# Performance work log

Measured on AMD Instinct MI355X. Metric: run time of the kernel, lower is better.

Reference implementation:

```python
import jax, jax.numpy as jnp
import numpy as np

NHEAD = 16
NUM_GROUPS = 4
EXPERTS_PER_GROUP = 2
LN_EPS = 1e-5


def _layernorm(x, g, b):
    mu = jnp.mean(x, axis=-1, keepdims=True)
    var = jnp.mean(jnp.square(x - mu), axis=-1, keepdims=True)
    return (x - mu) * jax.lax.rsqrt(var + LN_EPS) * g + b


def _mha(x, wi, bi, wo, bo):
    # torch nn.MultiheadAttention (batch_first): qkv = x @ in_proj_w.T + in_proj_b
    B, S, D = x.shape
    hd = D // NHEAD
    qkv = x @ wi.T + bi                      # [B,S,3D]
    q, k, v = jnp.split(qkv, 3, axis=-1)
    def heads(t):
        return t.reshape(B, S, NHEAD, hd).transpose(0, 2, 1, 3)  # [B,H,S,hd]
    q, k, v = heads(q), heads(k), heads(v)
    scores = jnp.einsum('bhqd,bhkd->bhqk', q, k) / jnp.sqrt(jnp.asarray(hd, x.dtype))
    attn = jax.nn.softmax(scores, axis=-1)
    o = jnp.einsum('bhqk,bhkd->bhqd', attn, v)
    o = o.transpose(0, 2, 1, 3).reshape(B, S, D)
    return o @ wo.T + bo


def _hier_moe(x, w_group, b_group, w_expert, b_expert, w1, b1, w2, b2):
    # Two-level top-1 routing: group gate -> expert gate within chosen group.
    B, S, D = x.shape
    xt = x.reshape(B * S, D)                 # [T,D]
    T = xt.shape[0]
    E = NUM_GROUPS * EXPERTS_PER_GROUP

    gp = jax.nn.softmax(xt @ w_group + b_group, axis=-1)          # [T,G]
    g_idx = jnp.argmax(gp, axis=-1)                                # [T]
    g_prob = jnp.max(gp, axis=-1)                                  # [T]

    elog = jnp.einsum('td,gde->tge', xt, w_expert) + b_expert      # [T,G,Epg]
    ep = jax.nn.softmax(elog, axis=-1)
    ep_sel = jnp.take_along_axis(ep, g_idx[:, None, None], axis=1)[:, 0, :]  # [T,Epg]
    e_idx_local = jnp.argmax(ep_sel, axis=-1)                      # [T]
    e_prob = jnp.max(ep_sel, axis=-1)                              # [T]

    flat_e = g_idx * EXPERTS_PER_GROUP + e_idx_local               # [T]
    combine = jax.nn.one_hot(flat_e, E, dtype=xt.dtype) * (g_prob * e_prob)[:, None]  # [T,E]

    # Dense dispatch (reference): run every expert on all tokens, combine with one-hot weights.
    h = jax.nn.relu(jnp.einsum('td,edf->etf', xt, w1) + b1[:, None, :])   # [E,T,Fff]
    y = jnp.einsum('etf,efd->etd', h, w2) + b2[:, None, :]                # [E,T,D]
    out = jnp.einsum('te,etd->td', combine, y)                            # [T,D]
    return out.reshape(B, S, D)


def setup_inputs() -> dict:
    key = jax.random.key(0)
    ks = jax.random.split(key, 8)
    B, S, D, F = 2, 1024, 1024, 2048
    G, Epg = NUM_GROUPS, EXPERTS_PER_GROUP
    E = G * Epg
    sc = lambda fan: 1.0 / np.sqrt(fan)
    return {
        'x': jax.random.normal(ks[0], (B, S, D), jnp.float32),
        'in_proj_w': jax.random.normal(ks[1], (3 * D, D), jnp.float32) * sc(D),
        'in_proj_b': jnp.zeros((3 * D,), jnp.float32),
        'out_proj_w': jax.random.normal(ks[2], (D, D), jnp.float32) * sc(D),
        'out_proj_b': jnp.zeros((D,), jnp.float32),
        'ln1_g': jnp.ones((D,), jnp.float32),
        'ln1_b': jnp.zeros((D,), jnp.float32),
        'ln2_g': jnp.ones((D,), jnp.float32),
        'ln2_b': jnp.zeros((D,), jnp.float32),
        'w_group': jax.random.normal(ks[3], (D, G), jnp.float32) * sc(D),
        'b_group': jnp.zeros((G,), jnp.float32),
        'w_expert': jax.random.normal(ks[4], (G, D, Epg), jnp.float32) * sc(D),
        'b_expert': jnp.zeros((G, Epg), jnp.float32),
        'w1': jax.random.normal(ks[5], (E, D, F), jnp.float32) * sc(D),
        'b1': jnp.zeros((E, F), jnp.float32),
        'w2': jax.random.normal(ks[6], (E, F, D), jnp.float32) * sc(F),
        'b2': jnp.zeros((E, D), jnp.float32),
    }


def reference(x, in_proj_w, in_proj_b, out_proj_w, out_proj_b,
              ln1_g, ln1_b, ln2_g, ln2_b,
              w_group, b_group, w_expert, b_expert, w1, b1, w2, b2):
    # Dropout p=0.1 is identity in eval mode.
    attn_out = _mha(x, in_proj_w, in_proj_b, out_proj_w, out_proj_b)
    x = _layernorm(x + attn_out, ln1_g, ln1_b)
    moe_out = _hier_moe(x, w_group, b_group, w_expert, b_expert, w1, b1, w2, b2)
    x = _layernorm(x + moe_out, ln2_g, ln2_b)
    return x
```

## Files before the change

### kernel.cpp

```cpp
#include <hip/hip_runtime.h>
#include <hip/hip_bf16.h>

#define TT 2048
#define DD 1024
#define FF 2048
#define SS 1024
#define NHD 16
#define HDD 64
#define NG 4
#define EPG 2
#define NE 8

#define QSC 0.18033688011112042f

typedef __attribute__((ext_vector_type(8))) short bf16x8;
typedef __attribute__((ext_vector_type(4))) float f32x4;
typedef __attribute__((ext_vector_type(4))) unsigned short ush4;

__device__ __forceinline__ unsigned short f2bf(float x) {
    unsigned int u = __float_as_uint(x);
    u = (u + 0x7fffu + ((u >> 16) & 1u)) >> 16;
    return (unsigned short)u;
}
__device__ __forceinline__ float bf2f(unsigned short h) {
    return __uint_as_float((unsigned int)h << 16);
}

__device__ __forceinline__ float wave_sum(float s) {
#pragma unroll
    for (int off = 32; off > 0; off >>= 1) s += __shfl_xor(s, off);
    return s;
}

__device__ __forceinline__ void gl16(const void* g, void* l) {
    auto gp = reinterpret_cast<const unsigned int __attribute__((address_space(1)))*>(
        (unsigned long long)g);
    auto lp = reinterpret_cast<unsigned int __attribute__((address_space(3)))*>(
        (unsigned int)(unsigned long long)l);
    __builtin_amdgcn_global_load_lds(gp, lp, 16, 0, 0);
}

__global__ __launch_bounds__(256) void split_bf16_kernel(
    const float* __restrict__ in, unsigned short* __restrict__ hi,
    unsigned short* __restrict__ lo, int n4)
{
    const int i = blockIdx.x * 256 + threadIdx.x;
    if (i >= n4) return;
    const float4 v = ((const float4*)in)[i];
    float vv[4] = {v.x, v.y, v.z, v.w};
    ush4 h, l;
#pragma unroll
    for (int j = 0; j < 4; ++j) {
        const unsigned short hb = f2bf(vv[j]);
        ((unsigned short*)&h)[j] = hb;
        ((unsigned short*)&l)[j] = f2bf(vv[j] - bf2f(hb));
    }
    ((ush4*)hi)[i] = h;
    ((ush4*)lo)[i] = l;
}

__global__ __launch_bounds__(256, 3) void gemm_split_kernel(
    const unsigned short* __restrict__ Ah, const unsigned short* __restrict__ Al,
    const unsigned short* __restrict__ Bh, const unsigned short* __restrict__ Bl,
    const float* __restrict__ bias, const float* __restrict__ resid,
    float* __restrict__ C, unsigned short* __restrict__ Chi,
    unsigned short* __restrict__ Clo, int qscale_n, int M, int N, int K)
{
    __shared__ unsigned short sAh[128 * 64];
    __shared__ unsigned short sAl[128 * 64];
    __shared__ unsigned short sBh[64 * 64];
    __shared__ unsigned short sBl[64 * 64];
    const int tid = threadIdx.x;
    const int lane = tid & 63, wid = tid >> 6;
    const int l15 = lane & 15, lg = lane >> 4;
    const int n0 = blockIdx.x << 6, m0 = blockIdx.y << 7;

    f32x4 acc[2][4];
#pragma unroll
    for (int mi = 0; mi < 2; ++mi)
#pragma unroll
        for (int ni = 0; ni < 4; ++ni) acc[mi][ni] = (f32x4){0.f, 0.f, 0.f, 0.f};

    for (int k0 = 0; k0 < K; k0 += 64) {
#pragma unroll
        for (int r = 0; r < 4; ++r) {
            const int s = (r << 8) + tid;
            const int row = s >> 3;
            const int cs = (s & 7) ^ (row & 7);
            const int lb = (s & ~63) << 3;
            const size_t ga = (size_t)(m0 + row) * K + k0 + (cs << 3);
            gl16(Ah + ga, &sAh[lb]);
            gl16(Al + ga, &sAl[lb]);
        }
#pragma unroll
        for (int r = 0; r < 2; ++r) {
            const int s = (r << 8) + tid;
            const int row = s >> 3;
            const int cs = (s & 7) ^ (row & 7);
            const int lb = (s & ~63) << 3;
            const size_t gb = (size_t)(n0 + row) * K + k0 + (cs << 3);
            gl16(Bh + gb, &sBh[lb]);
            gl16(Bl + gb, &sBl[lb]);
        }
        __syncthreads();
#pragma unroll
        for (int ks = 0; ks < 2; ++ks) {
            bf16x8 ah[2], al[2], bh[4], bl[4];
            const int ac = (ks << 2) + lg;
#pragma unroll
            for (int i = 0; i < 2; ++i) {
                const int ar = (wid << 5) + (i << 4) + l15;
                const int pa = ((ar << 3) | (ac ^ (ar & 7))) << 3;
                ah[i] = *(const bf16x8*)&sAh[pa];
                al[i] = *(const bf16x8*)&sAl[pa];
            }
#pragma unroll
            for (int i = 0; i < 4; ++i) {
                const int br = (i << 4) + l15;
                const int pb = ((br << 3) | (ac ^ (br & 7))) << 3;
                bh[i] = *(const bf16x8*)&sBh[pb];
                bl[i] = *(const bf16x8*)&sBl[pb];
            }
#pragma unroll
            for (int mi = 0; mi < 2; ++mi)
#pragma unroll
                for (int ni = 0; ni < 4; ++ni) {
                    acc[mi][ni] = __builtin_amdgcn_mfma_f32_16x16x32_bf16(ah[mi], bh[ni], acc[mi][ni], 0, 0, 0);
                    acc[mi][ni] = __builtin_amdgcn_mfma_f32_16x16x32_bf16(ah[mi], bl[ni], acc[mi][ni], 0, 0, 0);
                    acc[mi][ni] = __builtin_amdgcn_mfma_f32_16x16x32_bf16(al[mi], bh[ni], acc[mi][ni], 0, 0, 0);
                }
        }
        __syncthreads();
    }
#pragma unroll
    for (int mi = 0; mi < 2; ++mi)
#pragma unroll
        for (int ni = 0; ni < 4; ++ni)
#pragma unroll
            for (int r2 = 0; r2 < 4; ++r2) {
                const int m = m0 + (wid << 5) + (mi << 4) + (lg << 2) + r2;
                const int n = n0 + (ni << 4) + l15;
                float v = acc[mi][ni][r2] + bias[n];
                if (resid) v += resid[(size_t)m * N + n];
                const size_t idx = (size_t)m * N + n;
                if (Chi) {
                    if (n < qscale_n) v *= QSC;
                    const unsigned short hb = f2bf(v);
                    Chi[idx] = hb;
                    Clo[idx] = f2bf(v - bf2f(hb));
                } else {
                    C[idx] = v;
                }
            }
}

__global__ __launch_bounds__(256) void vtrans_kernel(
    const unsigned short* __restrict__ src, unsigned short* __restrict__ dst)
{
    __shared__ unsigned short tile[64][65];
    const int bh = blockIdx.y, b = bh >> 4, h = bh & 15;
    const int s0 = blockIdx.x << 6;
    const int tid = threadIdx.x;
#pragma unroll
    for (int r = 0; r < 2; ++r) {
        const int sl = tid + (r << 8);
        const int rr = sl >> 3, c8 = (sl & 7) << 3;
        const bf16x8 v = *(const bf16x8*)(src + (size_t)(b * SS + s0 + rr) * 3072 + 2048 + h * HDD + c8);
#pragma unroll
        for (int j = 0; j < 8; ++j) tile[rr][c8 + j] = ((const unsigned short*)&v)[j];
    }
    __syncthreads();
#pragma unroll
    for (int r = 0; r < 2; ++r) {
        const int sl = tid + (r << 8);
        const int d = sl >> 3, s8 = (sl & 7) << 3;
        bf16x8 o;
#pragma unroll
        for (int j = 0; j < 8; ++j) ((unsigned short*)&o)[j] = tile[s8 + j][d];
        *(bf16x8*)(dst + (size_t)(bh * HDD + d) * SS + s0 + s8) = o;
    }
}

__global__ __launch_bounds__(256, 4) void attn_mfma_kernel(
    const unsigned short* __restrict__ qh, const unsigned short* __restrict__ ql,
    const unsigned short* __restrict__ vth, const unsigned short* __restrict__ vtl,
    float* __restrict__ opart, float* __restrict__ mpart, float* __restrict__ lpart)
{
    __shared__ unsigned short sKh[4096], sKl[4096];
    __shared__ unsigned short sVh[4096], sVl[4096];
    const int bh = blockIdx.y, b = bh >> 4, h = bh & 15;
    const int q0 = blockIdx.x << 6;
    const int z = blockIdx.z;
    const int tid = threadIdx.x, lane = tid & 63, w = tid >> 6;
    const int l15 = lane & 15, lg = lane >> 4;

#pragma unroll
    for (int r = 0; r < 2; ++r) {
        const int s = (r << 8) + tid;
        const int row = s >> 3;
        const int cs = (s & 7) ^ (row & 7);
        const int lb = (s & ~63) << 3;
        const size_t gq = (size_t)(b * SS + q0 + row) * 3072 + h * HDD + (cs << 3);
        gl16(qh + gq, &sKh[lb]);
        gl16(ql + gq, &sKl[lb]);
    }
    __syncthreads();
    bf16x8 qah[2], qal[2];
#pragma unroll
    for (int ks = 0; ks < 2; ++ks) {
        const int ar = (w << 4) + l15;
        const int ac = (ks << 2) + lg;
        const int pa = ((ar << 3) | (ac ^ (ar & 7))) << 3;
        qah[ks] = *(const bf16x8*)&sKh[pa];
        qal[ks] = *(const bf16x8*)&sKl[pa];
    }
    __syncthreads();

    f32x4 accO[4];
#pragma unroll
    for (int nt = 0; nt < 4; ++nt) accO[nt] = (f32x4){0.f, 0.f, 0.f, 0.f};
    float m_run[4], l_run[4];
#pragma unroll
    for (int r2 = 0; r2 < 4; ++r2) { m_run[r2] = -3.0e38f; l_run[r2] = 0.f; }

    const int kvbeg = z << 9;
    for (int kv0 = kvbeg; kv0 < kvbeg + 512; kv0 += 64) {
#pragma unroll
        for (int r = 0; r < 2; ++r) {
            const int s = (r << 8) + tid;
            const int row = s >> 3;
            const int cs = (s & 7) ^ (row & 7);
            const int lb = (s & ~63) << 3;
            const size_t gk = (size_t)(b * SS + kv0 + row) * 3072 + DD + h * HDD + (cs << 3);
            gl16(qh + gk, &sKh[lb]);
            gl16(ql + gk, &sKl[lb]);
            const size_t gv = (size_t)(bh * HDD + row) * SS + kv0 + (cs << 3);
            gl16(vth + gv, &sVh[lb]);
            gl16(vtl + gv, &sVl[lb]);
        }
        __syncthreads();

        f32x4 sacc[4];
#pragma unroll
        for (int i = 0; i < 4; ++i) sacc[i] = (f32x4){0.f, 0.f, 0.f, 0.f};
        __builtin_amdgcn_s_setprio(1);
#pragma unroll
        for (int ks = 0; ks < 2; ++ks) {
            const int ac = (ks << 2) + lg;
#pragma unroll
            for (int i = 0; i < 4; ++i) {
                const int br = (i << 4) + l15;
                const int pb = ((br << 3) | (ac ^ (br & 7))) << 3;
                const bf16x8 kbh = *(const bf16x8*)&sKh[pb];
                const bf16x8 kbl = *(const bf16x8*)&sKl[pb];
                sacc[i] = __builtin_amdgcn_mfma_f32_16x16x32_bf16(qah[ks], kbh, sacc[i], 0, 0, 0);
                sacc[i] = __builtin_amdgcn_mfma_f32_16x16x32_bf16(qah[ks], kbl, sacc[i], 0, 0, 0);
                sacc[i] = __builtin_amdgcn_mfma_f32_16x16x32_bf16(qal[ks], kbh, sacc[i], 0, 0, 0);
            }
        }
        __builtin_amdgcn_s_setprio(0);
        __syncthreads();

#pragma unroll
        for (int r2 = 0; r2 < 4; ++r2) {
            float mx = fmaxf(fmaxf(sacc[0][r2], sacc[1][r2]), fmaxf(sacc[2][r2], sacc[3][r2]));
#pragma unroll
            for (int off = 1; off < 16; off <<= 1) mx = fmaxf(mx, __shfl_xor(mx, off));
            const float mn = fmaxf(m_run[r2], mx);
            const float corr = exp2f(m_run[r2] - mn);
            m_run[r2] = mn;
            float ls = 0.f;
#pragma unroll
            for (int nt = 0; nt < 4; ++nt) {
                const float p = exp2f(sacc[nt][r2] - mn);
                sacc[nt][r2] = p;
                ls += p;
            }
#pragma unroll
            for (int off = 1; off < 16; off <<= 1) ls += __shfl_xor(ls, off);
            l_run[r2] = l_run[r2] * corr + ls;
#pragma unroll
            for (int nt = 0; nt < 4; ++nt) accO[nt][r2] *= corr;
        }

#pragma unroll
        for (int nt = 0; nt < 4; ++nt)
#pragma unroll
            for (int r2 = 0; r2 < 4; ++r2) {
                const int qq = (w << 4) + (lg << 2) + r2;
                const int kv = (nt << 4) + l15;
                const int idx = (qq << 6) + ((((kv >> 3) ^ (qq & 7))) << 3) + (kv & 7);
                const float p = sacc[nt][r2];
                const unsigned short hb = (unsigned short)(__float_as_uint(p) >> 16);
                sKh[idx] = hb;
                sKl[idx] = (unsigned short)(__float_as_uint(p - bf2f(hb)) >> 16);
            }

        __builtin_amdgcn_s_setprio(1);
#pragma unroll
        for (int ks = 0; ks < 2; ++ks) {
            const int qq = (w << 4) + l15;
            const int slot = (ks << 2) + lg;
            const int pidx = (qq << 6) + ((slot ^ (qq & 7)) << 3);
            const bf16x8 pah = *(const bf16x8*)&sKh[pidx];
            const bf16x8 pal = *(const bf16x8*)&sKl[pidx];
            const int ac = (ks << 2) + lg;
#pragma unroll
            for (int nt = 0; nt < 4; ++nt) {
                const int dr = (nt << 4) + l15;
                const int pv = ((dr << 3) | (ac ^ (dr & 7))) << 3;
                const bf16x8 vbh = *(const bf16x8*)&sVh[pv];
                const bf16x8 vbl = *(const bf16x8*)&sVl[pv];
                accO[nt] = __builtin_amdgcn_mfma_f32_16x16x32_bf16(pah, vbh, accO[nt], 0, 0, 0);
                accO[nt] = __builtin_amdgcn_mfma_f32_16x16x32_bf16(pah, vbl, accO[nt], 0, 0, 0);
                accO[nt] = __builtin_amdgcn_mfma_f32_16x16x32_bf16(pal, vbh, accO[nt], 0, 0, 0);
            }
        }
        __builtin_amdgcn_s_setprio(0);
        __syncthreads();
    }

#pragma unroll
    for (int nt = 0; nt < 4; ++nt)
#pragma unroll
        for (int r2 = 0; r2 < 4; ++r2) {
            const int qq = q0 + (w << 4) + (lg << 2) + r2;
            const int dd = h * HDD + (nt << 4) + l15;
            opart[((size_t)z * TT + b * SS + qq) * DD + dd] = accO[nt][r2];
        }
    if (l15 == 0) {
#pragma unroll
        for (int r2 = 0; r2 < 4; ++r2) {
            const int qq = q0 + (w << 4) + (lg << 2) + r2;
            const int idx = z * (32 * SS) + bh * SS + qq;
            mpart[idx] = m_run[r2];
            lpart[idx] = l_run[r2];
        }
    }
}

__global__ __launch_bounds__(256) void attn_combine_kernel(
    const float* __restrict__ opart, const float* __restrict__ mpart,
    const float* __restrict__ lpart, unsigned short* __restrict__ ohi,
    unsigned short* __restrict__ olo)
{
    const int t = blockIdx.x;
    const int tid = threadIdx.x;
    const int b = t >> 10, q = t & 1023;
    const int d0 = tid << 2;
    const int bh = (b << 4) + (d0 >> 6);
    const int mi = bh * SS + q;
    const float m0 = mpart[mi], m1 = mpart[32 * SS + mi];
    const float l0 = lpart[mi], l1 = lpart[32 * SS + mi];
    const float m = fmaxf(m0, m1);
    const float e0 = exp2f(m0 - m), e1 = exp2f(m1 - m);
    const float inv = 1.0f / (l0 * e0 + l1 * e1);
    const float4 a = *(const float4*)(opart + (size_t)t * DD + d0);
    const float4 c = *(const float4*)(opart + (size_t)(TT + t) * DD + d0);
    const float vv[4] = { (a.x * e0 + c.x * e1) * inv, (a.y * e0 + c.y * e1) * inv,
                          (a.z * e0 + c.z * e1) * inv, (a.w * e0 + c.w * e1) * inv };
    ush4 hh, ll;
#pragma unroll
    for (int j = 0; j < 4; ++j) {
        const unsigned short hb = f2bf(vv[j]);
        hh[j] = hb;
        ll[j] = f2bf(vv[j] - bf2f(hb));
    }
    *(ush4*)(ohi + (size_t)t * DD + d0) = hh;
    *(ush4*)(olo + (size_t)t * DD + d0) = ll;
}

__global__ __launch_bounds__(256) void ln_kernel(
    const float* __restrict__ in, const float* __restrict__ gamma,
    const float* __restrict__ beta, float* __restrict__ outf)
{
    const int t = blockIdx.x;
    const int tid = threadIdx.x;
    __shared__ float red[8];
    const float4 v = ((const float4*)(in + (size_t)t * DD))[tid];
    float s = v.x + v.y + v.z + v.w;
    s = wave_sum(s);
    const int wid = tid >> 6, lane = tid & 63;
    if (lane == 0) red[wid] = s;
    __syncthreads();
    const float mu = (red[0] + red[1] + red[2] + red[3]) * (1.0f / DD);
    const float d0 = v.x - mu, d1 = v.y - mu, d2 = v.z - mu, d3 = v.w - mu;
    float q = d0 * d0 + d1 * d1 + d2 * d2 + d3 * d3;
    q = wave_sum(q);
    if (lane == 0) red[4 + wid] = q;
    __syncthreads();
    const float var = (red[4] + red[5] + red[6] + red[7]) * (1.0f / DD);
    const float rstd = 1.0f / sqrtf(var + 1e-5f);
    const float4 g4 = ((const float4*)gamma)[tid];
    const float4 b4 = ((const float4*)beta)[tid];
    float4 ov = { d0 * rstd * g4.x + b4.x, d1 * rstd * g4.y + b4.y,
                  d2 * rstd * g4.z + b4.z, d3 * rstd * g4.w + b4.w };
    ((float4*)(outf + (size_t)t * DD))[tid] = ov;
}

__global__ __launch_bounds__(256) void ln_route_kernel(
    const float* __restrict__ in, const float* __restrict__ gamma,
    const float* __restrict__ beta, float* __restrict__ outf,
    unsigned short* __restrict__ outb,
    const float* __restrict__ wg, const float* __restrict__ bg,
    const float* __restrict__ we, const float* __restrict__ be,
    int* __restrict__ eid, float* __restrict__ gate, int* __restrict__ counts)
{
    const int t = blockIdx.x;
    const int tid = threadIdx.x;
    __shared__ float red[8];
    __shared__ float red2[4][12];
    const float4 v = ((const float4*)(in + (size_t)t * DD))[tid];
    float s = v.x + v.y + v.z + v.w;
    s = wave_sum(s);
    const int wid = tid >> 6, lane = tid & 63;
    if (lane == 0) red[wid] = s;
    __syncthreads();
    const float mu = (red[0] + red[1] + red[2] + red[3]) * (1.0f / DD);
    const float d0 = v.x - mu, d1 = v.y - mu, d2 = v.z - mu, d3 = v.w - mu;
    float q = d0 * d0 + d1 * d1 + d2 * d2 + d3 * d3;
    q = wave_sum(q);
    if (lane == 0) red[4 + wid] = q;
    __syncthreads();
    const float var = (red[4] + red[5] + red[6] + red[7]) * (1.0f / DD);
    const float rstd = 1.0f / sqrtf(var + 1e-5f);
    const float4 g4 = ((const float4*)gamma)[tid];
    const float4 b4 = ((const float4*)beta)[tid];
    const float o0 = d0 * rstd * g4.x + b4.x;
    const float o1 = d1 * rstd * g4.y + b4.y;
    const float o2 = d2 * rstd * g4.z + b4.z;
    const float o3 = d3 * rstd * g4.w + b4.w;
    float4 ov = {o0, o1, o2, o3};
    ((float4*)(outf + (size_t)t * DD))[tid] = ov;
    ush4 wv = { f2bf(o0), f2bf(o1), f2bf(o2), f2bf(o3) };
    *(ush4*)(outb + (size_t)t * DD + (tid << 2)) = wv;

    float pz[12];
#pragma unroll
    for (int k = 0; k < 12; ++k) pz[k] = 0.f;
    const float xo[4] = {o0, o1, o2, o3};
#pragma unroll
    for (int j = 0; j < 4; ++j) {
        const int c = (tid << 2) + j;
        const float xv = xo[j];
        const float4 wgv = *(const float4*)(wg + c * NG);
        pz[0] = fmaf(xv, wgv.x, pz[0]);
        pz[1] = fmaf(xv, wgv.y, pz[1]);
        pz[2] = fmaf(xv, wgv.z, pz[2]);
        pz[3] = fmaf(xv, wgv.w, pz[3]);
#pragma unroll
        for (int g = 0; g < NG; ++g) {
            const float2 wev = *(const float2*)(we + ((size_t)g * DD + c) * EPG);
            pz[4 + 2 * g]     = fmaf(xv, wev.x, pz[4 + 2 * g]);
            pz[4 + 2 * g + 1] = fmaf(xv, wev.y, pz[4 + 2 * g + 1]);
        }
    }
#pragma unroll
    for (int k = 0; k < 12; ++k) pz[k] = wave_sum(pz[k]);
    if (lane == 0) {
#pragma unroll
        for (int k = 0; k < 12; ++k) red2[wid][k] = pz[k];
    }
    __syncthreads();
    if (tid == 0) {
        float zs[12];
#pragma unroll
        for (int k = 0; k < 12; ++k)
            zs[k] = red2[0][k] + red2[1][k] + red2[2][k] + red2[3][k];
        float z[NG];
#pragma unroll
        for (int g = 0; g < NG; ++g) z[g] = zs[g] + bg[g];
        int gi = 0; float zb = z[0];
#pragma unroll
        for (int g = 1; g < NG; ++g) if (z[g] > zb) { zb = z[g]; gi = g; }
        float se = 0.f;
#pragma unroll
        for (int g = 0; g < NG; ++g) se += __expf(z[g] - zb);
        const float gprob = 1.0f / se;
        float e0 = 0.f, e1 = 0.f;
#pragma unroll
        for (int g = 0; g < NG; ++g) {
            if (g == gi) {
                e0 = zs[4 + 2 * g] + be[g * EPG + 0];
                e1 = zs[4 + 2 * g + 1] + be[g * EPG + 1];
            }
        }
        const int ei = (e1 > e0) ? 1 : 0;
        const float ehi = ei ? e1 : e0, elo = ei ? e0 : e1;
        const float eprob = 1.0f / (1.0f + __expf(elo - ehi));
        eid[t] = gi * EPG + ei;
        gate[t] = gprob * eprob;
        atomicAdd(&counts[gi * EPG + ei], 1);
    }
}

__global__ void zero_counts_kernel(int* __restrict__ counts) {
    if (threadIdx.x < NE) counts[threadIdx.x] = 0;
}

__global__ void offsets_kernel(const int* __restrict__ counts, int* __restrict__ offs,
                               int* __restrict__ cursor) {
    if (threadIdx.x == 0) {
        int run = 0;
        for (int e = 0; e < NE; ++e) { offs[e] = run; cursor[e] = run; run += counts[e]; }
        offs[NE] = run;
    }
}

__global__ __launch_bounds__(256) void scatter_kernel(const int* __restrict__ eid,
                                                      int* __restrict__ cursor,
                                                      int* __restrict__ perm) {
    const int t = blockIdx.x * 256 + threadIdx.x;
    const int slot = atomicAdd(&cursor[eid[t]], 1);
    perm[slot] = t;
}

__global__ __launch_bounds__(256) void transpose_bf16_kernel(
    const float* __restrict__ in, unsigned short* __restrict__ out, int R, int C)
{
    __shared__ float tile[32][33];
    const int c0 = blockIdx.x << 5, r0 = blockIdx.y << 5;
    const size_t bo = (size_t)blockIdx.z * R * C;
    const int tc = threadIdx.x & 31, tr8 = threadIdx.x >> 5;
#pragma unroll
    for (int p = 0; p < 4; ++p) {
        const int rr = tr8 + (p << 3);
        tile[rr][tc] = in[bo + (size_t)(r0 + rr) * C + c0 + tc];
    }
    __syncthreads();
#pragma unroll
    for (int p = 0; p < 4; ++p) {
        const int rr = tr8 + (p << 3);
        out[bo + (size_t)(c0 + rr) * R + r0 + tc] = f2bf(tile[tc][rr]);
    }
}

__global__ __launch_bounds__(256, 4) void moe_gemm1_kernel(
    const unsigned short* __restrict__ x1b, const unsigned short* __restrict__ w1t,
    const float* __restrict__ b1, const int* __restrict__ offs,
    const int* __restrict__ perm, unsigned short* __restrict__ hbuf)
{
    const int e = blockIdx.y >> 5, mt = blockIdx.y & 31;
    const int row0 = offs[e] + (mt << 6);
    const int rend = offs[e + 1];
    if (row0 >= rend) return;
    const int valid = min(rend - row0, 64);
    const int n0 = blockIdx.x << 6;
    __shared__ unsigned short sA[2][64 * 64];
    __shared__ unsigned short sB[2][64 * 64];
    const int tid = threadIdx.x;
    const int lane = tid & 63, w = tid >> 6;
    const int l15 = lane & 15, lg = lane >> 4;

    size_t abase[2], bbase[2];
    int lbs[2];
#pragma unroll
    for (int r = 0; r < 2; ++r) {
        const int s = (r << 8) + tid;
        const int row = s >> 3;
        const int cs = (s & 7) ^ (row & 7);
        lbs[r] = (s & ~63) << 3;
        const int tk = perm[min(row0 + row, rend - 1)];
        abase[r] = (size_t)tk * DD + (cs << 3);
        bbase[r] = ((size_t)e * FF + n0 + row) * DD + (cs << 3);
    }

    f32x4 acc[4];
#pragma unroll
    for (int nt = 0; nt < 4; ++nt) acc[nt] = (f32x4){0.f, 0.f, 0.f, 0.f};

#pragma unroll
    for (int r = 0; r < 2; ++r) {
        gl16(x1b + abase[r], &sA[0][lbs[r]]);
        gl16(w1t + bbase[r], &sB[0][lbs[r]]);
    }
    __syncthreads();
    int cur = 0;
    for (int k0 = 0; k0 < DD; k0 += 64) {
        const int nxt = k0 + 64;
        if (nxt < DD) {
#pragma unroll
            for (int r = 0; r < 2; ++r) {
                gl16(x1b + abase[r] + nxt, &sA[cur ^ 1][lbs[r]]);
                gl16(w1t + bbase[r] + nxt, &sB[cur ^ 1][lbs[r]]);
            }
        }
#pragma unroll
        for (int ks = 0; ks < 2; ++ks) {
            const int ac = (ks << 2) + lg;
            const int ar = (w << 4) + l15;
            const int pa = ((ar << 3) | (ac ^ (ar & 7))) << 3;
            const bf16x8 a = *(const bf16x8*)&sA[cur][pa];
#pragma unroll
            for (int nt = 0; nt < 4; ++nt) {
                const int br = (nt << 4) + l15;
                const int pb = ((br << 3) | (ac ^ (br & 7))) << 3;
                acc[nt] = __builtin_amdgcn_mfma_f32_16x16x32_bf16(
                    a, *(const bf16x8*)&sB[cur][pb], acc[nt], 0, 0, 0);
            }
        }
        __syncthreads();
        cur ^= 1;
    }

    const float* bias = b1 + e * FF + n0;
    const int mbase = (w << 4) + (lg << 2);
#pragma unroll
    for (int nt = 0; nt < 4; ++nt) {
        const int n = (nt << 4) + l15;
#pragma unroll
        for (int r2 = 0; r2 < 4; ++r2) {
            const int m = mbase + r2;
            if (m < valid) {
                float v = fmaxf(acc[nt][r2] + bias[n], 0.f);
                hbuf[(size_t)(row0 + m) * FF + n0 + n] = f2bf(v);
            }
        }
    }
}

__global__ __launch_bounds__(256, 4) void moe_gemm2_kernel(
    const unsigned short* __restrict__ hbuf, const unsigned short* __restrict__ w2t,
    const int* __restrict__ offs, float* __restrict__ p0, float* __restrict__ p1)
{
    const int e = blockIdx.y >> 5, mt = blockIdx.y & 31;
    const int row0 = offs[e] + (mt << 6);
    const int rend = offs[e + 1];
    if (row0 >= rend) return;
    const int valid = min(rend - row0, 64);
    const int n0 = blockIdx.x << 6;
    const int z = blockIdx.z;
    float* __restrict__ pbuf = z ? p1 : p0;
    __shared__ unsigned short sA[2][64 * 64];
    __shared__ unsigned short sB[2][64 * 64];
    const int tid = threadIdx.x;
    const int lane = tid & 63, w = tid >> 6;
    const int l15 = lane & 15, lg = lane >> 4;

    size_t abase[2], bbase[2];
    int lbs[2];
#pragma unroll
    for (int r = 0; r < 2; ++r) {
        const int s = (r << 8) + tid;
        const int row = s >> 3;
        const int cs = (s & 7) ^ (row & 7);
        lbs[r] = (s & ~63) << 3;
        abase[r] = (size_t)(row0 + row) * FF + (cs << 3);
        bbase[r] = ((size_t)e * DD + n0 + row) * FF + (cs << 3);
    }

    f32x4 acc[4];
#pragma unroll
    for (int nt = 0; nt < 4; ++nt) acc[nt] = (f32x4){0.f, 0.f, 0.f, 0.f};

    const int kbeg = z << 10, kend = kbeg + 1024;
#pragma unroll
    for (int r = 0; r < 2; ++r) {
        gl16(hbuf + abase[r] + kbeg, &sA[0][lbs[r]]);
        gl16(w2t + bbase[r] + kbeg, &sB[0][lbs[r]]);
    }
    __syncthreads();
    int cur = 0;
    for (int k0 = kbeg; k0 < kend; k0 += 64) {
        const int nxt = k0 + 64;
        if (nxt < kend) {
#pragma unroll
            for (int r = 0; r < 2; ++r) {
                gl16(hbuf + abase[r] + nxt, &sA[cur ^ 1][lbs[r]]);
                gl16(w2t + bbase[r] + nxt, &sB[cur ^ 1][lbs[r]]);
            }
        }
#pragma unroll
        for (int ks = 0; ks < 2; ++ks) {
            const int ac = (ks << 2) + lg;
            const int ar = (w << 4) + l15;
            const int pa = ((ar << 3) | (ac ^ (ar & 7))) << 3;
            const bf16x8 a = *(const bf16x8*)&sA[cur][pa];
#pragma unroll
            for (int nt = 0; nt < 4; ++nt) {
                const int br = (nt << 4) + l15;
                const int pb = ((br << 3) | (ac ^ (br & 7))) << 3;
                acc[nt] = __builtin_amdgcn_mfma_f32_16x16x32_bf16(
                    a, *(const bf16x8*)&sB[cur][pb], acc[nt], 0, 0, 0);
            }
        }
        __syncthreads();
        cur ^= 1;
    }

    const int mbase = (w << 4) + (lg << 2);
#pragma unroll
    for (int nt = 0; nt < 4; ++nt) {
        const int n = (nt << 4) + l15;
#pragma unroll
        for (int r2 = 0; r2 < 4; ++r2) {
            const int m = mbase + r2;
            if (m < valid) pbuf[(size_t)(row0 + m) * DD + n0 + n] = acc[nt][r2];
        }
    }
}

__global__ __launch_bounds__(256) void moe2_combine_kernel(
    const float* __restrict__ p0, const float* __restrict__ p1,
    const int* __restrict__ offs, const int* __restrict__ perm,
    const float* __restrict__ gate, const float* __restrict__ b2,
    const float* __restrict__ x1, float* __restrict__ res2)
{
    const int s = blockIdx.x;
    const int tid = threadIdx.x;
    int e = 0;
#pragma unroll
    for (int g = 1; g < NE; ++g) e += (s >= offs[g]) ? 1 : 0;
    const int tk = perm[s];
    const float gt = gate[tk];
    const int c0 = tid << 2;
    const float4 a  = *(const float4*)(p0 + (size_t)s * DD + c0);
    const float4 b  = *(const float4*)(p1 + (size_t)s * DD + c0);
    const float4 bb = *(const float4*)(b2 + (size_t)e * DD + c0);
    const float4 xx = *(const float4*)(x1 + (size_t)tk * DD + c0);
    float4 o = { xx.x + gt * (a.x + b.x + bb.x), xx.y + gt * (a.y + b.y + bb.y),
                 xx.z + gt * (a.z + b.z + bb.z), xx.w + gt * (a.w + b.w + bb.w) };
    *(float4*)(res2 + (size_t)tk * DD + c0) = o;
}

extern "C" void kernel_launch(void* const* d_in, const int* in_sizes, int n_in,
                              void* d_out, int out_size, void* d_ws, size_t ws_size,
                              hipStream_t stream)
{
    (void)in_sizes; (void)n_in; (void)out_size; (void)ws_size;
    const float* x   = (const float*)d_in[0];
    const float* wi  = (const float*)d_in[1];
    const float* bi  = (const float*)d_in[2];
    const float* wo  = (const float*)d_in[3];
    const float* bo  = (const float*)d_in[4];
    const float* g1  = (const float*)d_in[5];
    const float* be1 = (const float*)d_in[6];
    const float* g2  = (const float*)d_in[7];
    const float* be2 = (const float*)d_in[8];
    const float* wgr = (const float*)d_in[9];
    const float* bgr = (const float*)d_in[10];
    const float* wex = (const float*)d_in[11];
    const float* bex = (const float*)d_in[12];
    const float* w1  = (const float*)d_in[13];
    const float* b1  = (const float*)d_in[14];
    const float* w2  = (const float*)d_in[15];
    const float* b2  = (const float*)d_in[16];
    float* out = (float*)d_out;

    char* ws = (char*)d_ws;
    unsigned short* qkvh  = (unsigned short*)(ws + 0);
    unsigned short* qkvl  = (unsigned short*)(ws + 12582912);
    unsigned short* hbuf  = (unsigned short*)(ws + 0);
    float* res2           = (float*)(ws + 8388608);
    unsigned short* vth   = (unsigned short*)(ws + 25165824);
    unsigned short* vtl   = (unsigned short*)(ws + 29360128);
    float* res1           = (float*)(ws + 33554432);
    float* x1             = (float*)(ws + 41943040);
    unsigned short* x1b   = (unsigned short*)(ws + 50331648);
    unsigned short* w1t   = (unsigned short*)(ws + 54525952);
    unsigned short* w2t   = (unsigned short*)(ws + 88080384);
    char* misc = ws + 121634816;
    int*   eid    = (int*)(misc);
    float* gate   = (float*)(misc + 8192);
    int*   perm   = (int*)(misc + 16384);
    int*   counts = (int*)(misc + 24576);
    int*   offs   = (int*)(misc + 24640);
    int*   cursor = (int*)(misc + 24704);

    unsigned short* xs_hi = (unsigned short*)(ws + 33554432);
    unsigned short* xs_lo = (unsigned short*)(ws + 33554432 + 4194304);
    unsigned short* wi_hi = (unsigned short*)(ws + 54525952);
    unsigned short* wi_lo = (unsigned short*)(ws + 54525952 + 6291456);
    unsigned short* o_hi  = (unsigned short*)(ws + 41943040);
    unsigned short* o_lo  = (unsigned short*)(ws + 41943040 + 4194304);
    unsigned short* wo_hi = (unsigned short*)(ws + 88080384);
    unsigned short* wo_lo = (unsigned short*)(ws + 88080384 + 2097152);

    float* opart = (float*)(ws + 54525952);
    float* mpart = (float*)(ws + 54525952 + 16777216);
    float* lpart = (float*)(ws + 54525952 + 17039360);

    float* mp0 = (float*)(ws + 16777216);
    float* mp1 = (float*)(ws + 25165824);

    zero_counts_kernel<<<dim3(1), dim3(64), 0, stream>>>(counts);

    split_bf16_kernel<<<dim3((TT * DD / 4 + 255) / 256), dim3(256), 0, stream>>>(x, xs_hi, xs_lo, TT * DD / 4);
    split_bf16_kernel<<<dim3((3 * DD * DD / 4 + 255) / 256), dim3(256), 0, stream>>>(wi, wi_hi, wi_lo, 3 * DD * DD / 4);
    gemm_split_kernel<<<dim3(3 * DD / 64, TT / 128), dim3(256), 0, stream>>>(
        xs_hi, xs_lo, wi_hi, wi_lo, bi, (const float*)nullptr,
        (float*)nullptr, qkvh, qkvl, DD, TT, 3 * DD, DD);

    vtrans_kernel<<<dim3(SS / 64, 2 * NHD), dim3(256), 0, stream>>>(qkvh, vth);
    vtrans_kernel<<<dim3(SS / 64, 2 * NHD), dim3(256), 0, stream>>>(qkvl, vtl);

    attn_mfma_kernel<<<dim3(SS / 64, 2 * NHD, 2), dim3(256), 0, stream>>>(
        qkvh, qkvl, vth, vtl, opart, mpart, lpart);
    attn_combine_kernel<<<dim3(TT), dim3(256), 0, stream>>>(opart, mpart, lpart, o_hi, o_lo);

    split_bf16_kernel<<<dim3((DD * DD / 4 + 255) / 256), dim3(256), 0, stream>>>(wo, wo_hi, wo_lo, DD * DD / 4);
    gemm_split_kernel<<<dim3(DD / 64, TT / 128), dim3(256), 0, stream>>>(
        o_hi, o_lo, wo_hi, wo_lo, bo, x,
        res1, (unsigned short*)nullptr, (unsigned short*)nullptr, 0, TT, DD, DD);

    ln_route_kernel<<<dim3(TT), dim3(256), 0, stream>>>(
        res1, g1, be1, x1, x1b, wgr, bgr, wex, bex, eid, gate, counts);
    offsets_kernel<<<dim3(1), dim3(64), 0, stream>>>(counts, offs, cursor);
    scatter_kernel<<<dim3(TT / 256), dim3(256), 0, stream>>>(eid, cursor, perm);

    transpose_bf16_kernel<<<dim3(FF / 32, DD / 32, NE), dim3(256), 0, stream>>>(w1, w1t, DD, FF);
    transpose_bf16_kernel<<<dim3(DD / 32, FF / 32, NE), dim3(256), 0, stream>>>(w2, w2t, FF, DD);

    moe_gemm1_kernel<<<dim3(FF / 64, NE * 32), dim3(256), 0, stream>>>(x1b, w1t, b1, offs, perm, hbuf);
    moe_gemm2_kernel<<<dim3(DD / 64, NE * 32, 2), dim3(256), 0, stream>>>(hbuf, w2t, offs, mp0, mp1);
    moe2_combine_kernel<<<dim3(TT), dim3(256), 0, stream>>>(mp0, mp1, offs, perm, gate, b2, x1, res2);

    ln_kernel<<<dim3(TT), dim3(256), 0, stream>>>(res2, g2, be2, out);
}
```

Baseline: 291.5 us.

## Split-K the output projection and transpose the score MFMA to simplify softmax

```diff
diff --git a/kernel.cpp b/kernel.cpp
--- a/kernel.cpp
+++ b/kernel.cpp
@@ -74,6 +74,9 @@
     const int lane = tid & 63, wid = tid >> 6;
     const int l15 = lane & 15, lg = lane >> 4;
     const int n0 = blockIdx.x << 6, m0 = blockIdx.y << 7;
+    const int kper = K / gridDim.z;
+    const int kbeg = blockIdx.z * kper, kend = kbeg + kper;
+    float* __restrict__ Cz = C ? (C + (size_t)blockIdx.z * M * N) : C;
 
     f32x4 acc[2][4];
 #pragma unroll
@@ -81,7 +84,7 @@
 #pragma unroll
         for (int ni = 0; ni < 4; ++ni) acc[mi][ni] = (f32x4){0.f, 0.f, 0.f, 0.f};
 
-    for (int k0 = 0; k0 < K; k0 += 64) {
+    for (int k0 = kbeg; k0 < kend; k0 += 64) {
 #pragma unroll
         for (int r = 0; r < 4; ++r) {
             const int s = (r << 8) + tid;
@@ -140,7 +143,8 @@
             for (int r2 = 0; r2 < 4; ++r2) {
                 const int m = m0 + (wid << 5) + (mi << 4) + (lg << 2) + r2;
                 const int n = n0 + (ni << 4) + l15;
-                float v = acc[mi][ni][r2] + bias[n];
+                float v = acc[mi][ni][r2];
+                if (bias) v += bias[n];
                 if (resid) v += resid[(size_t)m * N + n];
                 const size_t idx = (size_t)m * N + n;
                 if (Chi) {
@@ -149,7 +153,7 @@
                     Chi[idx] = hb;
                     Clo[idx] = f2bf(v - bf2f(hb));
                 } else {
-                    C[idx] = v;
+                    Cz[idx] = v;
                 }
             }
 }
@@ -219,9 +223,7 @@
     f32x4 accO[4];
 #pragma unroll
     for (int nt = 0; nt < 4; ++nt) accO[nt] = (f32x4){0.f, 0.f, 0.f, 0.f};
-    float m_run[4], l_run[4];
-#pragma unroll
-    for (int r2 = 0; r2 < 4; ++r2) { m_run[r2] = -3.0e38f; l_run[r2] = 0.f; }
+    float m_run = -3.0e38f, l_run = 0.f;
 
     const int kvbeg = z << 9;
     for (int kv0 = kvbeg; kv0 < kvbeg + 512; kv0 += 64) {
@@ -253,48 +255,53 @@
                 const int pb = ((br << 3) | (ac ^ (br & 7))) << 3;
                 const bf16x8 kbh = *(const bf16x8*)&sKh[pb];
                 const bf16x8 kbl = *(const bf16x8*)&sKl[pb];
-                sacc[i] = __builtin_amdgcn_mfma_f32_16x16x32_bf16(qah[ks], kbh, sacc[i], 0, 0, 0);
-                sacc[i] = __builtin_amdgcn_mfma_f32_16x16x32_bf16(qah[ks], kbl, sacc[i], 0, 0, 0);
-                sacc[i] = __builtin_amdgcn_mfma_f32_16x16x32_bf16(qal[ks], kbh, sacc[i], 0, 0, 0);
+                sacc[i] = __builtin_amdgcn_mfma_f32_16x16x32_bf16(kbh, qah[ks], sacc[i], 0, 0, 0);
+                sacc[i] = __builtin_amdgcn_mfma_f32_16x16x32_bf16(kbh, qal[ks], sacc[i], 0, 0, 0);
+                sacc[i] = __builtin_amdgcn_mfma_f32_16x16x32_bf16(kbl, qah[ks], sacc[i], 0, 0, 0);
             }
         }
         __builtin_amdgcn_s_setprio(0);
         __syncthreads();
 
-#pragma unroll
-        for (int r2 = 0; r2 < 4; ++r2) {
-            float mx = fmaxf(fmaxf(sacc[0][r2], sacc[1][r2]), fmaxf(sacc[2][r2], sacc[3][r2]));
-#pragma unroll
-            for (int off = 1; off < 16; off <<= 1) mx = fmaxf(mx, __shfl_xor(mx, off));
-            const float mn = fmaxf(m_run[r2], mx);
-            const float corr = exp2f(m_run[r2] - mn);
-            m_run[r2] = mn;
-            float ls = 0.f;
-#pragma unroll
-            for (int nt = 0; nt < 4; ++nt) {
-                const float p = exp2f(sacc[nt][r2] - mn);
-                sacc[nt][r2] = p;
+        float mx = sacc[0][0];
+#pragma unroll
+        for (int i = 0; i < 4; ++i)
+#pragma unroll
+            for (int r2 = 0; r2 < 4; ++r2) mx = fmaxf(mx, sacc[i][r2]);
+        mx = fmaxf(mx, __shfl_xor(mx, 16));
+        mx = fmaxf(mx, __shfl_xor(mx, 32));
+        const float mn = fmaxf(m_run, mx);
+        const float corr = exp2f(m_run - mn);
+        m_run = mn;
+        float ls = 0.f;
+        const int qrow = (w << 4) | l15;
+#pragma unroll
+        for (int i = 0; i < 4; ++i) {
+            ush4 hp, lp;
+#pragma unroll
+            for (int r2 = 0; r2 < 4; ++r2) {
+                const float p = exp2f(sacc[i][r2] - mn);
                 ls += p;
-            }
-#pragma unroll
-            for (int off = 1; off < 16; off <<= 1) ls += __shfl_xor(ls, off);
-            l_run[r2] = l_run[r2] * corr + ls;
-#pragma unroll
-            for (int nt = 0; nt < 4; ++nt) accO[nt][r2] *= corr;
-        }
-
+                const unsigned short hb = (unsigned short)(__float_as_uint(p) >> 16);
+                hp[r2] = hb;
+                lp[r2] = (unsigned short)(__float_as_uint(p - bf2f(hb)) >> 16);
+            }
+            const int kvb = (i << 4) + (lg << 2);
+            const int idx = (qrow << 6) + (((kvb >> 3) ^ (qrow & 7)) << 3) + (kvb & 7);
+            *(ush4*)&sKh[idx] = hp;
+            *(ush4*)&sKl[idx] = lp;
+        }
+        ls += __shfl_xor(ls, 16);
+        ls += __shfl_xor(ls, 32);
+        l_run = l_run * corr + ls;
+        float c4[4];
+#pragma unroll
+        for (int r2 = 0; r2 < 4; ++r2)
+            c4[r2] = __shfl(corr, (lane & 48) | ((lg << 2) + r2));
 #pragma unroll
         for (int nt = 0; nt < 4; ++nt)
 #pragma unroll
-            for (int r2 = 0; r2 < 4; ++r2) {
-                const int qq = (w << 4) + (lg << 2) + r2;
-                const int kv = (nt << 4) + l15;
-                const int idx = (qq << 6) + ((((kv >> 3) ^ (qq & 7))) << 3) + (kv & 7);
-                const float p = sacc[nt][r2];
-                const unsigned short hb = (unsigned short)(__float_as_uint(p) >> 16);
-                sKh[idx] = hb;
-                sKl[idx] = (unsigned short)(__float_as_uint(p - bf2f(hb)) >> 16);
-            }
+            for (int r2 = 0; r2 < 4; ++r2) accO[nt][r2] *= c4[r2];
 
         __builtin_amdgcn_s_setprio(1);
 #pragma unroll
@@ -328,14 +335,11 @@
             const int dd = h * HDD + (nt << 4) + l15;
             opart[((size_t)z * TT + b * SS + qq) * DD + dd] = accO[nt][r2];
         }
-    if (l15 == 0) {
-#pragma unroll
-        for (int r2 = 0; r2 < 4; ++r2) {
-            const int qq = q0 + (w << 4) + (lg << 2) + r2;
-            const int idx = z * (32 * SS) + bh * SS + qq;
-            mpart[idx] = m_run[r2];
-            lpart[idx] = l_run[r2];
-        }
+    if (lane < 16) {
+        const int qq = q0 + (w << 4) + lane;
+        const int idx = z * (32 * SS) + bh * SS + qq;
+        mpart[idx] = m_run;
+        lpart[idx] = l_run;
     }
 }
 
@@ -399,9 +403,10 @@
 }
 
 __global__ __launch_bounds__(256) void ln_route_kernel(
-    const float* __restrict__ in, const float* __restrict__ gamma,
-    const float* __restrict__ beta, float* __restrict__ outf,
-    unsigned short* __restrict__ outb,
+    const float* __restrict__ x, const float* __restrict__ p0,
+    const float* __restrict__ p1, const float* __restrict__ bo,
+    const float* __restrict__ gamma, const float* __restrict__ beta,
+    float* __restrict__ outf, unsigned short* __restrict__ outb,
     const float* __restrict__ wg, const float* __restrict__ bg,
     const float* __restrict__ we, const float* __restrict__ be,
     int* __restrict__ eid, float* __restrict__ gate, int* __restrict__ counts)
@@ -410,7 +415,12 @@
     const int tid = threadIdx.x;
     __shared__ float red[8];
     __shared__ float red2[4][12];
-    const float4 v = ((const float4*)(in + (size_t)t * DD))[tid];
+    const float4 xv = ((const float4*)(x + (size_t)t * DD))[tid];
+    const float4 a4 = ((const float4*)(p0 + (size_t)t * DD))[tid];
+    const float4 c4v = ((const float4*)(p1 + (size_t)t * DD))[tid];
+    const float4 bo4 = ((const float4*)bo)[tid];
+    const float4 v = { xv.x + a4.x + c4v.x + bo4.x, xv.y + a4.y + c4v.y + bo4.y,
+                       xv.z + a4.z + c4v.z + bo4.z, xv.w + a4.w + c4v.w + bo4.w };
     float s = v.x + v.y + v.z + v.w;
     s = wave_sum(s);
     const int wid = tid >> 6, lane = tid & 63;
@@ -442,17 +452,17 @@
 #pragma unroll
     for (int j = 0; j < 4; ++j) {
         const int c = (tid << 2) + j;
-        const float xv = xo[j];
+        const float xvv = xo[j];
         const float4 wgv = *(const float4*)(wg + c * NG);
-        pz[0] = fmaf(xv, wgv.x, pz[0]);
-        pz[1] = fmaf(xv, wgv.y, pz[1]);
-        pz[2] = fmaf(xv, wgv.z, pz[2]);
-        pz[3] = fmaf(xv, wgv.w, pz[3]);
+        pz[0] = fmaf(xvv, wgv.x, pz[0]);
+        pz[1] = fmaf(xvv, wgv.y, pz[1]);
+        pz[2] = fmaf(xvv, wgv.z, pz[2]);
+        pz[3] = fmaf(xvv, wgv.w, pz[3]);
 #pragma unroll
         for (int g = 0; g < NG; ++g) {
             const float2 wev = *(const float2*)(we + ((size_t)g * DD + c) * EPG);
-            pz[4 + 2 * g]     = fmaf(xv, wev.x, pz[4 + 2 * g]);
-            pz[4 + 2 * g + 1] = fmaf(xv, wev.y, pz[4 + 2 * g + 1]);
+            pz[4 + 2 * g]     = fmaf(xvv, wev.x, pz[4 + 2 * g]);
+            pz[4 + 2 * g + 1] = fmaf(xvv, wev.y, pz[4 + 2 * g + 1]);
         }
     }
 #pragma unroll
@@ -754,7 +764,6 @@
     float* res2           = (float*)(ws + 8388608);
     unsigned short* vth   = (unsigned short*)(ws + 25165824);
     unsigned short* vtl   = (unsigned short*)(ws + 29360128);
-    float* res1           = (float*)(ws + 33554432);
     float* x1             = (float*)(ws + 41943040);
     unsigned short* x1b   = (unsigned short*)(ws + 50331648);
     unsigned short* w1t   = (unsigned short*)(ws + 54525952);
@@ -780,6 +789,8 @@
     float* mpart = (float*)(ws + 54525952 + 16777216);
     float* lpart = (float*)(ws + 54525952 + 17039360);
 
+    float* oproj = (float*)(ws + 0);
+
     float* mp0 = (float*)(ws + 16777216);
     float* mp1 = (float*)(ws + 25165824);
 
@@ -787,7 +798,7 @@
 
     split_bf16_kernel<<<dim3((TT * DD / 4 + 255) / 256), dim3(256), 0, stream>>>(x, xs_hi, xs_lo, TT * DD / 4);
     split_bf16_kernel<<<dim3((3 * DD * DD / 4 + 255) / 256), dim3(256), 0, stream>>>(wi, wi_hi, wi_lo, 3 * DD * DD / 4);
-    gemm_split_kernel<<<dim3(3 * DD / 64, TT / 128), dim3(256), 0, stream>>>(
+    gemm_split_kernel<<<dim3(3 * DD / 64, TT / 128, 1), dim3(256), 0, stream>>>(
         xs_hi, xs_lo, wi_hi, wi_lo, bi, (const float*)nullptr,
         (float*)nullptr, qkvh, qkvl, DD, TT, 3 * DD, DD);
 
@@ -799,12 +810,13 @@
     attn_combine_kernel<<<dim3(TT), dim3(256), 0, stream>>>(opart, mpart, lpart, o_hi, o_lo);
 
     split_bf16_kernel<<<dim3((DD * DD / 4 + 255) / 256), dim3(256), 0, stream>>>(wo, wo_hi, wo_lo, DD * DD / 4);
-    gemm_split_kernel<<<dim3(DD / 64, TT / 128), dim3(256), 0, stream>>>(
-        o_hi, o_lo, wo_hi, wo_lo, bo, x,
-        res1, (unsigned short*)nullptr, (unsigned short*)nullptr, 0, TT, DD, DD);
+    gemm_split_kernel<<<dim3(DD / 64, TT / 128, 2), dim3(256), 0, stream>>>(
+        o_hi, o_lo, wo_hi, wo_lo, (const float*)nullptr, (const float*)nullptr,
+        oproj, (unsigned short*)nullptr, (unsigned short*)nullptr, 0, TT, DD, DD);
 
     ln_route_kernel<<<dim3(TT), dim3(256), 0, stream>>>(
-        res1, g1, be1, x1, x1b, wgr, bgr, wex, bex, eid, gate, counts);
+        x, oproj, oproj + (size_t)TT * DD, bo, g1, be1, x1, x1b,
+        wgr, bgr, wex, bex, eid, gate, counts);
     offsets_kernel<<<dim3(1), dim3(64), 0, stream>>>(counts, offs, cursor);
     scatter_kernel<<<dim3(TT / 256), dim3(256), 0, stream>>>(eid, cursor, perm);
 
```

New measurement: 273.7 us. 6.1% less time.
